# Kernel optimization log

Hardware: AMD Instinct MI355X
Metric: run time of the kernel (lower is better)

Reference implementation:

```python
import jax, jax.numpy as jnp
import numpy as np

B, T, D, KDIM = 256, 512, 256, 256

def setup_inputs() -> dict:
    key = jax.random.key(0)
    k1, k2, k3 = jax.random.split(key, 3)
    inputs = jax.random.normal(k1, (B, T, D), dtype=jnp.float32)
    # glorot-style scaling for stability of the recurrence
    U = jax.random.normal(k2, (D, KDIM), dtype=jnp.float32) * (1.0 / np.sqrt(D))
    W = jax.random.normal(k3, (KDIM, KDIM), dtype=jnp.float32) * (1.0 / np.sqrt(KDIM))
    b = jnp.zeros((KDIM,), dtype=jnp.float32)
    return {"inputs": inputs, "U": U, "W": W, "b": b}

def reference(inputs, U, W, b):
    # vanilla RNN: h_t = tanh(x_t U + h_{t-1} W + b); returns final hidden state
    xU = jnp.einsum('btd,dk->btk', inputs, U) + b  # precompute input projection [B,T,K]

    def step(h, xu_t):
        h = jnp.tanh(xu_t + h @ W)
        return h, None

    h0 = jnp.zeros((inputs.shape[0], W.shape[0]), dtype=inputs.dtype)
    h_final, _ = jax.lax.scan(step, h0, jnp.swapaxes(xU, 0, 1))  # scan over time
    # original keras code keeps a singleton time axis on the state: [B,1,K]
    return h_final[:, None, :]
```

## Files before the change

### kernel.cpp

```cpp
#include <hip/hip_runtime.h>
#include <hip/hip_bf16.h>


typedef _Float16 half8_t __attribute__((ext_vector_type(8)));
typedef _Float16 half2_t __attribute__((ext_vector_type(2)));
typedef float    float4_t __attribute__((ext_vector_type(4)));

#define MFMA16(a, b, c) __builtin_amdgcn_mfma_f32_16x16x32_f16((a), (b), (c), 0, 0, 0)

__device__ __forceinline__ half2_t pk_h2(float a, float b) {
    auto r = __builtin_amdgcn_cvt_pkrtz(a, b);
    return __builtin_bit_cast(half2_t, r);
}

__device__ __forceinline__ float fast_tanh(float x) {
    float e = __builtin_amdgcn_exp2f(2.8853900817779268f * x);
    return 1.0f - 2.0f * __builtin_amdgcn_rcpf(e + 1.0f);
}

__global__ void transpose_u(const float* __restrict__ U, _Float16* __restrict__ Ut) {
    int id = blockIdx.x * 256 + threadIdx.x;
    int d = id >> 8, n = id & 255;
    Ut[n * 264 + d] = (_Float16)U[id];
}

__global__ __launch_bounds__(256, 2) void xu_gemm(
    const float* __restrict__ x,
    const _Float16* __restrict__ Ut,
    const float* __restrict__ bias,
    half2_t* __restrict__ xu)
{
    __shared__ char lds[61440];
    const int tid = threadIdx.x;
    const int lane = tid & 63, w = tid >> 6, l15 = lane & 15, q = lane >> 4;
    const int bx = blockIdx.x;
    const size_t m0 = (size_t)bx * 128;

    float4 ar[4];
    uint4  br[4];

    auto loadA = [&](int it) {
#pragma unroll
        for (int i = 0; i < 4; ++i) {
            int u = tid + 256 * i, row = u >> 3, seg = u & 7;
            ar[i] = *(const float4*)(x + (m0 + row) * 256 + it * 32 + seg * 4);
        }
    };
    auto loadB = [&](int it) {
#pragma unroll
        for (int i = 0; i < 4; ++i) {
            int u = tid + 256 * i, p = u >> 2, seg = u & 3;
            int c = 32 * (p >> 5) + 2 * (p & 15) + ((p >> 4) & 1);
            br[i] = *(const uint4*)((const char*)Ut + c * 528 + it * 64 + seg * 16);
        }
    };
    auto writeAB = [&](int s) {
        char* As = lds + s * 10240;
        char* Bs = lds + 20480 + s * 20480;
#pragma unroll
        for (int i = 0; i < 4; ++i) {
            int u = tid + 256 * i, row = u >> 3, seg = u & 7;
            half2_t p0 = pk_h2(ar[i].x, ar[i].y);
            half2_t p1 = pk_h2(ar[i].z, ar[i].w);
            uint2 v;
            v.x = __builtin_bit_cast(unsigned, p0);
            v.y = __builtin_bit_cast(unsigned, p1);
            *(uint2*)(As + row * 80 + seg * 8) = v;
        }
#pragma unroll
        for (int i = 0; i < 4; ++i) {
            int u = tid + 256 * i, p = u >> 2, seg = u & 3;
            *(uint4*)(Bs + p * 80 + seg * 16) = br[i];
        }
    };

    float4_t acc[32];
#pragma unroll
    for (int i = 0; i < 32; ++i) { acc[i][0] = 0.f; acc[i][1] = 0.f; acc[i][2] = 0.f; acc[i][3] = 0.f; }

    loadA(0); loadB(0); writeAB(0);
    __syncthreads();

    for (int it = 0; it < 8; ++it) {
        if (it < 7) { loadA(it + 1); loadB(it + 1); }
        const char* As = lds + (it & 1) * 10240;
        const char* Bs = lds + 20480 + (it & 1) * 20480;
        half8_t af[2];
#pragma unroll
        for (int ms = 0; ms < 2; ++ms)
            af[ms] = *(const half8_t*)(As + (32 * w + 16 * ms + l15) * 80 + q * 16);
#pragma unroll
        for (int ns = 0; ns < 16; ++ns) {
            half8_t bf = *(const half8_t*)(Bs + (16 * ns + l15) * 80 + q * 16);
            acc[ns * 2 + 0] = MFMA16(af[0], bf, acc[ns * 2 + 0]);
            acc[ns * 2 + 1] = MFMA16(af[1], bf, acc[ns * 2 + 1]);
        }
        if (it < 7) writeAB((it + 1) & 1);
        __syncthreads();
    }

#pragma unroll
    for (int ms = 0; ms < 2; ++ms)
#pragma unroll
        for (int j = 0; j < 8; ++j) {
            const int c = 32 * j + 2 * l15;
            const float2 bb = *(const float2*)(bias + c);
#pragma unroll
            for (int i = 0; i < 4; ++i) {
                float v0 = acc[(2 * j) * 2 + ms][i] + bb.x;
                float v1 = acc[(2 * j + 1) * 2 + ms][i] + bb.y;
                half2_t p = pk_h2(v0, v1);
                int m_g = bx * 128 + 32 * w + 16 * ms + q * 4 + i;
                xu[(size_t)m_g * 128 + (c >> 1)] = p;
            }
        }
}

__global__ __launch_bounds__(512, 2) void rnn_scan(
    const half2_t* __restrict__ xu,
    const float* __restrict__ W,
    float* __restrict__ out)
{
    __shared__ char lds[16896];
    const int tid = threadIdx.x;
    const int lane = tid & 63, w = tid >> 6, l15 = lane & 15, q = lane >> 4;
    const int blk = blockIdx.x;
    const int c0 = 32 * w + 2 * l15;

    half8_t wf[2][8];
#pragma unroll
    for (int tt = 0; tt < 2; ++tt)
#pragma unroll
        for (int c = 0; c < 8; ++c) {
            half8_t f;
#pragma unroll
            for (int j = 0; j < 8; ++j) {
                int k = 32 * c + q * 8 + j;
                f[j] = (_Float16)W[k * 256 + c0 + tt];
            }
            wf[tt][c] = f;
        }

    for (int i = tid; i < 16896 / 4; i += 512) ((int*)lds)[i] = 0;

    const int rowg0 = 16 * blk + q * 4;
    const int colh = c0 >> 1;

    half2_t xr[4][4];
#pragma unroll
    for (int p = 0; p < 4; ++p)
#pragma unroll
        for (int i = 0; i < 4; ++i)
            xr[p][i] = xu[((rowg0 + i) * 512 + p) * 128 + colh];

    __syncthreads();

    char* const hbuf0 = (char*)lds;
    char* const hbuf1 = (char*)lds + 8448;

    for (int t4 = 0; t4 < 512; t4 += 4) {
#pragma unroll
        for (int p = 0; p < 4; ++p) {
            const int t = t4 + p;

            float4_t a0a, a1a, a0b, a1b;
#pragma unroll
            for (int i = 0; i < 4; ++i) {
                a0a[i] = (float)xr[p][i][0];
                a1a[i] = (float)xr[p][i][1];
                a0b[i] = 0.f; a1b[i] = 0.f;
            }

            const char* hcur = (t & 1) ? hbuf1 : hbuf0;
            half8_t af[8];
#pragma unroll
            for (int c = 0; c < 8; ++c)
                af[c] = *(const half8_t*)(hcur + l15 * 528 + c * 64 + q * 16);

            const int tn = (t + 4 <= 511) ? (t + 4) : 511;
#pragma unroll
            for (int i = 0; i < 4; ++i)
                xr[p][i] = xu[((rowg0 + i) * 512 + tn) * 128 + colh];

#pragma unroll
            for (int c = 0; c < 4; ++c) {
                a0a = MFMA16(af[2 * c],     wf[0][2 * c],     a0a);
                a1a = MFMA16(af[2 * c],     wf[1][2 * c],     a1a);
                a0b = MFMA16(af[2 * c + 1], wf[0][2 * c + 1], a0b);
                a1b = MFMA16(af[2 * c + 1], wf[1][2 * c + 1], a1b);
            }

            if (t == 511) {
#pragma unroll
                for (int i = 0; i < 4; ++i) {
                    float v0 = fast_tanh(a0a[i] + a0b[i]);
                    float v1 = fast_tanh(a1a[i] + a1b[i]);
                    float2 st; st.x = v0; st.y = v1;
                    *(float2*)(&out[(rowg0 + i) * 256 + c0]) = st;
                }
            } else {
                char* hnext = ((t + 1) & 1) ? hbuf1 : hbuf0;
#pragma unroll
                for (int i = 0; i < 4; ++i) {
                    float v0 = fast_tanh(a0a[i] + a0b[i]);
                    float v1 = fast_tanh(a1a[i] + a1b[i]);
                    *(half2_t*)(hnext + (q * 4 + i) * 528 + c0 * 2) = pk_h2(v0, v1);
                }
            }
            __syncthreads();
        }
    }
}

extern "C" void kernel_launch(void* const* d_in, const int* in_sizes, int n_in,
                              void* d_out, int out_size, void* d_ws, size_t ws_size,
                              hipStream_t stream) {
    const float* x = (const float*)d_in[0];
    const float* U = (const float*)d_in[1];
    const float* W = (const float*)d_in[2];
    const float* b = (const float*)d_in[3];
    float* out = (float*)d_out;

    char* ws = (char*)d_ws;
    _Float16* Ut = (_Float16*)ws;
    half2_t*  xu = (half2_t*)(ws + 262144);

    transpose_u<<<256, 256, 0, stream>>>(U, Ut);
    xu_gemm<<<1024, 256, 0, stream>>>(x, Ut, b, xu);
    rnn_scan<<<16, 512, 0, stream>>>(xu, W, out);
}
```

Measured before the change: 525.8 us.

## Halve rnn_scan block to four waves, each computing two column groups

The recurrent scan now runs 256 threads per block instead of 512. Each wave owns 64 output columns (two 32-column groups), and W fragments are held in registers for both groups. The MFMA chains are regrouped so the first group's tanh can overlap the second group's MFMAs, and the per-step barrier now synchronises fewer waves. In exchange each wave does twice the MFMA work on the serial critical path and register pressure roughly doubles.

```diff
diff --git a/kernel.cpp b/kernel.cpp
--- a/kernel.cpp
+++ b/kernel.cpp
@@ -116,7 +116,7 @@
         }
 }
 
-__global__ __launch_bounds__(512, 2) void rnn_scan(
+__global__ __launch_bounds__(256, 1) void rnn_scan(
     const half2_t* __restrict__ xu,
     const float* __restrict__ W,
     float* __restrict__ out)
@@ -125,33 +125,37 @@
     const int tid = threadIdx.x;
     const int lane = tid & 63, w = tid >> 6, l15 = lane & 15, q = lane >> 4;
     const int blk = blockIdx.x;
-    const int c0 = 32 * w + 2 * l15;
-
-    half8_t wf[2][8];
-#pragma unroll
-    for (int tt = 0; tt < 2; ++tt)
-#pragma unroll
-        for (int c = 0; c < 8; ++c) {
-            half8_t f;
-#pragma unroll
-            for (int j = 0; j < 8; ++j) {
-                int k = 32 * c + q * 8 + j;
-                f[j] = (_Float16)W[k * 256 + c0 + tt];
-            }
-            wf[tt][c] = f;
-        }
-
-    for (int i = tid; i < 16896 / 4; i += 512) ((int*)lds)[i] = 0;
+    const int c0 = 64 * w + 2 * l15;
+
+    half8_t wf[2][2][8];
+#pragma unroll
+    for (int u = 0; u < 2; ++u)
+#pragma unroll
+        for (int tt = 0; tt < 2; ++tt)
+#pragma unroll
+            for (int c = 0; c < 8; ++c) {
+                half8_t f;
+#pragma unroll
+                for (int j = 0; j < 8; ++j) {
+                    int k = 32 * c + q * 8 + j;
+                    f[j] = (_Float16)W[k * 256 + c0 + 32 * u + tt];
+                }
+                wf[u][tt][c] = f;
+            }
+
+    for (int i = tid; i < 16896 / 4; i += 256) ((int*)lds)[i] = 0;
 
     const int rowg0 = 16 * blk + q * 4;
-    const int colh = c0 >> 1;
-
-    half2_t xr[4][4];
+    const int ch0 = 32 * w + l15;
+
+    half2_t xr[4][2][4];
 #pragma unroll
     for (int p = 0; p < 4; ++p)
 #pragma unroll
-        for (int i = 0; i < 4; ++i)
-            xr[p][i] = xu[((rowg0 + i) * 512 + p) * 128 + colh];
+        for (int u = 0; u < 2; ++u)
+#pragma unroll
+            for (int i = 0; i < 4; ++i)
+                xr[p][u][i] = xu[((size_t)(rowg0 + i) * 512 + p) * 128 + ch0 + 16 * u];
 
     __syncthreads();
 
@@ -163,12 +167,13 @@
         for (int p = 0; p < 4; ++p) {
             const int t = t4 + p;
 
-            float4_t a0a, a1a, a0b, a1b;
+            float4_t acc00, acc01, acc10, acc11;
 #pragma unroll
             for (int i = 0; i < 4; ++i) {
-                a0a[i] = (float)xr[p][i][0];
-                a1a[i] = (float)xr[p][i][1];
-                a0b[i] = 0.f; a1b[i] = 0.f;
+                acc00[i] = (float)xr[p][0][i][0];
+                acc01[i] = (float)xr[p][0][i][1];
+                acc10[i] = (float)xr[p][1][i][0];
+                acc11[i] = (float)xr[p][1][i][1];
             }
 
             const char* hcur = (t & 1) ? hbuf1 : hbuf0;
@@ -179,32 +184,43 @@
 
             const int tn = (t + 4 <= 511) ? (t + 4) : 511;
 #pragma unroll
-            for (int i = 0; i < 4; ++i)
-                xr[p][i] = xu[((rowg0 + i) * 512 + tn) * 128 + colh];
-
-#pragma unroll
-            for (int c = 0; c < 4; ++c) {
-                a0a = MFMA16(af[2 * c],     wf[0][2 * c],     a0a);
-                a1a = MFMA16(af[2 * c],     wf[1][2 * c],     a1a);
-                a0b = MFMA16(af[2 * c + 1], wf[0][2 * c + 1], a0b);
-                a1b = MFMA16(af[2 * c + 1], wf[1][2 * c + 1], a1b);
+            for (int u = 0; u < 2; ++u)
+#pragma unroll
+                for (int i = 0; i < 4; ++i)
+                    xr[p][u][i] = xu[((size_t)(rowg0 + i) * 512 + tn) * 128 + ch0 + 16 * u];
+
+#pragma unroll
+            for (int c = 0; c < 8; ++c) {
+                acc00 = MFMA16(af[c], wf[0][0][c], acc00);
+                acc01 = MFMA16(af[c], wf[0][1][c], acc01);
+            }
+            float v0[4], v1[4];
+#pragma unroll
+            for (int i = 0; i < 4; ++i) {
+                v0[i] = fast_tanh(acc00[i]);
+                v1[i] = fast_tanh(acc01[i]);
+            }
+#pragma unroll
+            for (int c = 0; c < 8; ++c) {
+                acc10 = MFMA16(af[c], wf[1][0][c], acc10);
+                acc11 = MFMA16(af[c], wf[1][1][c], acc11);
             }
 
             if (t == 511) {
 #pragma unroll
                 for (int i = 0; i < 4; ++i) {
-                    float v0 = fast_tanh(a0a[i] + a0b[i]);
-                    float v1 = fast_tanh(a1a[i] + a1b[i]);
-                    float2 st; st.x = v0; st.y = v1;
-                    *(float2*)(&out[(rowg0 + i) * 256 + c0]) = st;
+                    float2 s0; s0.x = v0[i]; s0.y = v1[i];
+                    *(float2*)(&out[(rowg0 + i) * 256 + c0]) = s0;
+                    float2 s1; s1.x = fast_tanh(acc10[i]); s1.y = fast_tanh(acc11[i]);
+                    *(float2*)(&out[(rowg0 + i) * 256 + c0 + 32]) = s1;
                 }
             } else {
                 char* hnext = ((t + 1) & 1) ? hbuf1 : hbuf0;
 #pragma unroll
                 for (int i = 0; i < 4; ++i) {
-                    float v0 = fast_tanh(a0a[i] + a0b[i]);
-                    float v1 = fast_tanh(a1a[i] + a1b[i]);
-                    *(half2_t*)(hnext + (q * 4 + i) * 528 + c0 * 2) = pk_h2(v0, v1);
+                    *(half2_t*)(hnext + (q * 4 + i) * 528 + c0 * 2) = pk_h2(v0[i], v1[i]);
+                    *(half2_t*)(hnext + (q * 4 + i) * 528 + (c0 + 32) * 2) =
+                        pk_h2(fast_tanh(acc10[i]), fast_tanh(acc11[i]));
                 }
             }
             __syncthreads();
@@ -227,5 +243,5 @@
 
     transpose_u<<<256, 256, 0, stream>>>(U, Ut);
     xu_gemm<<<1024, 256, 0, stream>>>(x, Ut, b, xu);
-    rnn_scan<<<16, 512, 0, stream>>>(xu, W, out);
-}
+    rnn_scan<<<16, 256, 0, stream>>>(xu, W, out);
+}
```

Result: slower. 581.8 us (+10.7%).
